# Performance work log

Measured on AMD Instinct MI355X. Metric: run time of the kernel, lower is better.

## Reference

```python
import jax, jax.numpy as jnp
import numpy as np

NUM_HEAD = 16
FEAT_DIM = 1024
HEAD_DIM = FEAT_DIM // NUM_HEAD  # 64
MAX_SEQ_LEN = 2048
BATCH = 2


def setup_inputs() -> dict:
    key = jax.random.key(0)
    ks = jax.random.split(key, 6)
    x = jax.random.normal(ks[0], (BATCH, MAX_SEQ_LEN, FEAT_DIM), dtype=jnp.float32)
    # xavier_uniform: limit = sqrt(6/(fan_in+fan_out)); torch Linear weight is [out, in]
    def xavier(k, out_f, in_f):
        lim = float(np.sqrt(6.0 / (in_f + out_f)))
        return jax.random.uniform(k, (out_f, in_f), dtype=jnp.float32, minval=-lim, maxval=lim)
    W1 = xavier(ks[1], HEAD_DIM, HEAD_DIM)          # attn_mlp[0].weight
    b1 = jnp.zeros((HEAD_DIM,), dtype=jnp.float32)
    W2 = xavier(ks[2], MAX_SEQ_LEN, HEAD_DIM)       # attn_mlp[2].weight
    b2 = jnp.zeros((MAX_SEQ_LEN,), dtype=jnp.float32)
    Wv = xavier(ks[3], FEAT_DIM, FEAT_DIM)          # value_linear.weight (no bias)
    Wo = xavier(ks[4], FEAT_DIM, FEAT_DIM)          # output_linear.weight (no bias)
    return {"x": x, "W1": W1, "b1": b1, "W2": W2, "b2": b2, "Wv": Wv, "Wo": Wo}


def _split_head(t):
    b, n, _ = t.shape
    return t.reshape(b, n, NUM_HEAD, HEAD_DIM).transpose(0, 2, 1, 3)  # [b,h,n,d]


def reference(x, W1, b1, W2, b2, Wv, Wo):
    # value projection (dropout is identity in eval / p=0)
    value = x @ Wv.T                                   # [b,n,F]
    vh = _split_head(value)                            # [b,h,n,d]
    xh = _split_head(x)                                # [b,h,n,d]
    # per-head MLP -> dense attention logits [b,h,n,max_seq_len]
    hid = jax.nn.relu(jnp.einsum('bhnd,ed->bhne', xh, W1) + b1)
    logits = jnp.einsum('bhne,me->bhnm', hid, W2) + b2
    attn = jax.nn.softmax(logits, axis=-1)             # [b,h,n,m]
    out_h = jnp.einsum('bhnm,bhmd->bhnd', attn, vh)    # m == seq_len
    b_, h_, n_, d_ = out_h.shape
    out = out_h.transpose(0, 2, 1, 3).reshape(b_, n_, FEAT_DIM)
    return out @ Wo.T
```

## Files before the change

### kernel.cpp

```cpp
#include <hip/hip_runtime.h>
#include <hip/hip_bf16.h>
#include <math.h>
#include <stdint.h>


typedef __attribute__((ext_vector_type(8))) short bf16x8;
typedef __attribute__((ext_vector_type(4))) float f32x4;
typedef __attribute__((ext_vector_type(16))) float f32x16;

#define LOG2E 1.4426950408889634f

__device__ __forceinline__ unsigned short f2bf(float f) {
  union { float f; unsigned u; } v; v.f = f;
  unsigned r = v.u + 0x7FFFu + ((v.u >> 16) & 1u);
  return (unsigned short)(r >> 16);
}

__global__ __launch_bounds__(256) void prep_all(const float* __restrict__ x,
                                                const float* __restrict__ Wv,
                                                const float* __restrict__ Wo,
                                                const float* __restrict__ W2,
                                                const float* __restrict__ W1,
                                                const float* __restrict__ b2,
                                                unsigned short* __restrict__ xb,
                                                unsigned short* __restrict__ wvb,
                                                unsigned short* __restrict__ wob,
                                                unsigned short* __restrict__ w2b,
                                                unsigned short* __restrict__ w1b,
                                                float* __restrict__ b2l) {
  int bid = blockIdx.x;
  if (bid == 2048) {
    int i = threadIdx.x;
#pragma unroll
    for (int t = 0; t < 8; ++t) {
      int k = i * 8 + t;
      b2l[k] = b2[k] * LOG2E;
    }
    return;
  }
  int stride = 2048 * 256;
  for (int q = bid * 256 + threadIdx.x; q < 1606656; q += stride) {
    const float* s; unsigned short* d; int o;
    if (q < 1048576)      { s = x;  d = xb;  o = q; }
    else {
      int q2 = q - 1048576;
      if (q2 < 262144)      { s = Wv; d = wvb; o = q2; }
      else if (q2 < 524288) { s = Wo; d = wob; o = q2 - 262144; }
      else if (q2 < 557056) { s = W2; d = w2b; o = q2 - 524288; }
      else                  { s = W1; d = w1b; o = q2 - 557056; }
    }
    float4 v = *(const float4*)(s + (size_t)o * 4);
    uint2 u;
    u.x = (unsigned)f2bf(v.x) | ((unsigned)f2bf(v.y) << 16);
    u.y = (unsigned)f2bf(v.z) | ((unsigned)f2bf(v.w) << 16);
    *(uint2*)(d + (size_t)o * 4) = u;
  }
}

__device__ __forceinline__ void stage64(const char* g, size_t ldbytes, char* lds,
                                        int w, int lane) {
#pragma unroll
  for (int t = 0; t < 2; ++t) {
    int row  = w * 16 + t * 8 + (lane >> 3);
    int csrc = (lane & 7) ^ (lane >> 3);
    const char* src = g + (size_t)row * ldbytes + (csrc << 4);
    char* dst = lds + ((w * 2 + t) << 10);
    __builtin_amdgcn_global_load_lds((const __attribute__((address_space(1))) void*)src,
                                     (__attribute__((address_space(3))) void*)dst,
                                     16, 0, 0);
  }
}

__device__ __forceinline__ void stage8(const char* g, size_t ldbytes, char* lds_,
                                       int w, int lane) {
  int row  = w * 8 + (lane >> 3);
  int csrc = (lane & 7) ^ (lane >> 3);
  const char* src = g + (size_t)row * ldbytes + (csrc << 4);
  char* dst = lds_ + (w << 10);
  __builtin_amdgcn_global_load_lds((const __attribute__((address_space(1))) void*)src,
                                   (__attribute__((address_space(3))) void*)dst,
                                   16, 0, 0);
}

__device__ __forceinline__ bf16x8 rdfrag32(const char* lds, int row, int chunk) {
  int c = chunk ^ (row & 7);
  return *(const bf16x8*)(lds + row * 128 + (c << 4));
}

__device__ __forceinline__ f32x16 loadb16(const float* p) {
  f32x16 r;
#pragma unroll
  for (int qd = 0; qd < 4; ++qd) {
    float4 v = *(const float4*)(p + qd * 8);
    r[qd * 4 + 0] = v.x; r[qd * 4 + 1] = v.y; r[qd * 4 + 2] = v.z; r[qd * 4 + 3] = v.w;
  }
  return r;
}

__device__ __forceinline__ bf16x8 pk_swap(float r0, float r1, float r2, float r3,
                                          float r4, float r5, float r6, float r7) {
  unsigned a, b, c, d;
  asm("v_cvt_pk_bf16_f32 %0, %1, %2" : "=v"(a) : "v"(r0), "v"(r1));
  asm("v_cvt_pk_bf16_f32 %0, %1, %2" : "=v"(b) : "v"(r4), "v"(r5));
  asm("v_cvt_pk_bf16_f32 %0, %1, %2" : "=v"(c) : "v"(r2), "v"(r3));
  asm("v_cvt_pk_bf16_f32 %0, %1, %2" : "=v"(d) : "v"(r6), "v"(r7));
  asm("v_permlane32_swap_b32 %0, %1" : "+v"(a), "+v"(b));
  asm("v_permlane32_swap_b32 %0, %1" : "+v"(c), "+v"(d));
  union { unsigned u[4]; bf16x8 v; } r;
  r.u[0] = a; r.u[1] = c; r.u[2] = b; r.u[3] = d;
  return r.v;
}

template<int MODE>
__global__ __launch_bounds__(256) void gemm12864(const unsigned short* __restrict__ A,
                                                 const unsigned short* __restrict__ B,
                                                 void* __restrict__ C, int K) {
  __shared__ __attribute__((aligned(16))) char As[2][16384];
  __shared__ __attribute__((aligned(16))) char Bs[2][8192];
  int tid = threadIdx.x, w = tid >> 6, lane = tid & 63;
  int l31 = lane & 31, hi = lane >> 5;
  int wr = w >> 1, wc = w & 1;
  int bm = blockIdx.x, bn = blockIdx.y;
  const char* Ab = (const char*)A + (size_t)bm * 128 * (K * 2);
  const char* Bb = (const char*)B + (size_t)bn * 64 * (K * 2);
  size_t ld = (size_t)K * 2;

  f32x16 acc0 = {}, acc1 = {};
  stage64(Ab, ld, As[0], w, lane);
  stage64(Ab + 64 * ld, ld, As[0] + 8192, w, lane);
  stage64(Bb, ld, Bs[0], w, lane);
  __syncthreads();

  int nst = K >> 6;
  for (int kk = 0; kk < nst; ++kk) {
    int cur = kk & 1;
    if (kk + 1 < nst) {
      const char* An = Ab + (size_t)(kk + 1) * 128;
      const char* Bn = Bb + (size_t)(kk + 1) * 128;
      stage64(An, ld, As[cur ^ 1], w, lane);
      stage64(An + 64 * ld, ld, As[cur ^ 1] + 8192, w, lane);
      stage64(Bn, ld, Bs[cur ^ 1], w, lane);
    }
    __builtin_amdgcn_s_setprio(1);
#pragma unroll
    for (int ks = 0; ks < 4; ++ks) {
      bf16x8 a0 = rdfrag32(As[cur], wr * 64 + l31, ks * 2 + hi);
      bf16x8 a1 = rdfrag32(As[cur], wr * 64 + 32 + l31, ks * 2 + hi);
      bf16x8 b0 = rdfrag32(Bs[cur], wc * 32 + l31, ks * 2 + hi);
      acc0 = __builtin_amdgcn_mfma_f32_32x32x16_bf16(a0, b0, acc0, 0, 0, 0);
      acc1 = __builtin_amdgcn_mfma_f32_32x32x16_bf16(a1, b0, acc1, 0, 0, 0);
    }
    __builtin_amdgcn_s_setprio(0);
    __syncthreads();
  }

  if (MODE == 0) {
    unsigned short* vt = (unsigned short*)C;
    int d = wc * 32 + l31;
#pragma unroll
    for (int i = 0; i < 2; ++i) {
      f32x16 a = i ? acc1 : acc0;
      int rowb = bm * 128 + wr * 64 + i * 32;
#pragma unroll
      for (int qd = 0; qd < 4; ++qd) {
        int m0 = rowb + qd * 8 + hi * 4;
        int bb = m0 >> 11, n = m0 & 2047;
        int r0 = qd * 4;
        uint2 u;
        u.x = (unsigned)f2bf(a[r0]) | ((unsigned)f2bf(a[r0 + 1]) << 16);
        u.y = (unsigned)f2bf(a[r0 + 2]) | ((unsigned)f2bf(a[r0 + 3]) << 16);
        *(uint2*)(vt + ((size_t)((bb * 16 + bn) * 64 + d)) * 2048 + n) = u;
      }
    }
  } else {
    float* Cf = (float*)C;
    int rb = bm * 128 + wr * 64, cb = bn * 64 + wc * 32;
#pragma unroll
    for (int r = 0; r < 16; ++r) {
      int row = (r & 3) + 8 * (r >> 2) + 4 * hi;
      Cf[(size_t)(rb + row) * 1024 + cb + l31]      = acc0[r];
      Cf[(size_t)(rb + 32 + row) * 1024 + cb + l31] = acc1[r];
    }
  }
}

__global__ __launch_bounds__(512, 2) void flash_kernel(const unsigned short* __restrict__ xb,
                                                       const unsigned short* __restrict__ w1b,
                                                       const float* __restrict__ b1,
                                                       const unsigned short* __restrict__ w2b,
                                                       const float* __restrict__ b2l,
                                                       const unsigned short* __restrict__ vt,
                                                       unsigned short* __restrict__ aout) {
  __shared__ __attribute__((aligned(16))) char lds[65536];
  int tid = threadIdx.x, w = tid >> 6, lane = tid & 63;
  int wq = w & 3, grp = w >> 2;
  int l31 = lane & 31, hi = lane >> 5;
  int f = blockIdx.x;
  int swz = ((f & 7) << 6) | (f >> 3);
  int qt = swz & 15, bh = swz >> 4;
  int b = bh >> 4, h = bh & 15;

  const char* px = (const char*)(xb + ((size_t)(b * 2048 + qt * 128)) * 1024 + h * 64);
  stage8(px, 2048, lds, w, lane);
  stage8(px + (size_t)64 * 2048, 2048, lds + 8192, w, lane);
  stage8((const char*)w1b, 128, lds + 32768, w, lane);
  __syncthreads();

  f32x16 h0 = loadb16(b1 + hi * 4);
  f32x16 h1 = loadb16(b1 + 32 + hi * 4);
  {
    const char* xt = lds + (wq >> 1) * 8192;
    int xr = (wq & 1) * 32 + l31;
#pragma unroll
    for (int ks = 0; ks < 4; ++ks) {
      bf16x8 xf = rdfrag32(xt, xr, ks * 2 + hi);
      bf16x8 wf0 = rdfrag32(lds + 32768, l31, ks * 2 + hi);
      h0 = __builtin_amdgcn_mfma_f32_32x32x16_bf16(wf0, xf, h0, 0, 0, 0);
      bf16x8 wf1 = rdfrag32(lds + 32768, 32 + l31, ks * 2 + hi);
      h1 = __builtin_amdgcn_mfma_f32_32x32x16_bf16(wf1, xf, h1, 0, 0, 0);
    }
  }
#pragma unroll
  for (int i = 0; i < 16; ++i) {
    h0[i] = fmaxf(h0[i], 0.f) * LOG2E;
    h1[i] = fmaxf(h1[i], 0.f) * LOG2E;
  }
  bf16x8 qb[4];
  qb[0] = pk_swap(h0[0], h0[1], h0[2], h0[3], h0[4], h0[5], h0[6], h0[7]);
  qb[1] = pk_swap(h0[8], h0[9], h0[10], h0[11], h0[12], h0[13], h0[14], h0[15]);
  qb[2] = pk_swap(h1[0], h1[1], h1[2], h1[3], h1[4], h1[5], h1[6], h1[7]);
  qb[3] = pk_swap(h1[8], h1[9], h1[10], h1[11], h1[12], h1[13], h1[14], h1[15]);
  __syncthreads();

  const char* vtb = (const char*)vt + (size_t)bh * 64 * 4096;
#pragma unroll
  for (int t = 0; t < 4; ++t) {
    stage8((const char*)w2b + (size_t)t * 8192, 128, lds + t * 8192, w, lane);
    stage8(vtb + (size_t)t * 128, 4096, lds + 32768 + t * 8192, w, lane);
  }
  f32x16 oA = {}, oB = {};
  float lrs0 = 0.f, lrs1 = 0.f, lrs2 = 0.f, lrs3 = 0.f;
  __syncthreads();

  for (int s = 0; s < 16; ++s) {
    int mt = 2 * s + grp;
    const char* Kc = lds + (mt & 3) * 8192;
    const char* Vc = lds + 32768 + (mt & 3) * 8192;

    f32x16 s0, s1;
#pragma unroll
    for (int qd = 0; qd < 4; ++qd) {
      f32x4 p0 = *(const f32x4*)(b2l + mt * 64 + qd * 8 + hi * 4);
      f32x4 p1 = *(const f32x4*)(b2l + mt * 64 + 32 + qd * 8 + hi * 4);
#pragma unroll
      for (int j = 0; j < 4; ++j) {
        s0[qd * 4 + j] = p0[j];
        s1[qd * 4 + j] = p1[j];
      }
    }
    __builtin_amdgcn_s_setprio(1);
#pragma unroll
    for (int kt = 0; kt < 4; ++kt) {
      bf16x8 kf0 = rdfrag32(Kc, l31, kt * 2 + hi);
      s0 = __builtin_amdgcn_mfma_f32_32x32x16_bf16(kf0, qb[kt], s0, 0, 0, 0);
      bf16x8 kf1 = rdfrag32(Kc, 32 + l31, kt * 2 + hi);
      s1 = __builtin_amdgcn_mfma_f32_32x32x16_bf16(kf1, qb[kt], s1, 0, 0, 0);
    }
    __builtin_amdgcn_s_setprio(0);
#pragma unroll
    for (int i = 0; i < 16; ++i) {
      float t0, t1;
      asm("v_exp_f32 %0, %1" : "=v"(t0) : "v"(s0[i]));
      asm("v_exp_f32 %0, %1" : "=v"(t1) : "v"(s1[i]));
      s0[i] = t0; s1[i] = t1;
      if ((i & 3) == 0) { lrs0 += t0; lrs0 += t1; }
      else if ((i & 3) == 1) { lrs1 += t0; lrs1 += t1; }
      else if ((i & 3) == 2) { lrs2 += t0; lrs2 += t1; }
      else { lrs3 += t0; lrs3 += t1; }
    }
    bf16x8 pa0 = pk_swap(s0[0], s0[1], s0[2], s0[3], s0[4], s0[5], s0[6], s0[7]);
    bf16x8 pa1 = pk_swap(s0[8], s0[9], s0[10], s0[11], s0[12], s0[13], s0[14], s0[15]);
    bf16x8 pa2 = pk_swap(s1[0], s1[1], s1[2], s1[3], s1[4], s1[5], s1[6], s1[7]);
    bf16x8 pa3 = pk_swap(s1[8], s1[9], s1[10], s1[11], s1[12], s1[13], s1[14], s1[15]);
    __builtin_amdgcn_s_setprio(1);
    {
      bf16x8 vf;
      vf = rdfrag32(Vc, l31, 0 + hi);
      oA = __builtin_amdgcn_mfma_f32_32x32x16_bf16(pa0, vf, oA, 0, 0, 0);
      vf = rdfrag32(Vc, 32 + l31, 0 + hi);
      oB = __builtin_amdgcn_mfma_f32_32x32x16_bf16(pa0, vf, oB, 0, 0, 0);
      vf = rdfrag32(Vc, l31, 2 + hi);
      oA = __builtin_amdgcn_mfma_f32_32x32x16_bf16(pa1, vf, oA, 0, 0, 0);
      vf = rdfrag32(Vc, 32 + l31, 2 + hi);
      oB = __builtin_amdgcn_mfma_f32_32x32x16_bf16(pa1, vf, oB, 0, 0, 0);
      vf = rdfrag32(Vc, l31, 4 + hi);
      oA = __builtin_amdgcn_mfma_f32_32x32x16_bf16(pa2, vf, oA, 0, 0, 0);
      vf = rdfrag32(Vc, 32 + l31, 4 + hi);
      oB = __builtin_amdgcn_mfma_f32_32x32x16_bf16(pa2, vf, oB, 0, 0, 0);
      vf = rdfrag32(Vc, l31, 6 + hi);
      oA = __builtin_amdgcn_mfma_f32_32x32x16_bf16(pa3, vf, oA, 0, 0, 0);
      vf = rdfrag32(Vc, 32 + l31, 6 + hi);
      oB = __builtin_amdgcn_mfma_f32_32x32x16_bf16(pa3, vf, oB, 0, 0, 0);
    }
    __builtin_amdgcn_s_setprio(0);
    __syncthreads();
    if (s < 14) {
      int t0 = 2 * s + 4, t1 = 2 * s + 5;
      stage8((const char*)w2b + (size_t)t0 * 8192, 128, lds + (t0 & 3) * 8192, w, lane);
      stage8(vtb + (size_t)t0 * 128, 4096, lds + 32768 + (t0 & 3) * 8192, w, lane);
      stage8((const char*)w2b + (size_t)t1 * 8192, 128, lds + (t1 & 3) * 8192, w, lane);
      stage8(vtb + (size_t)t1 * 128, 4096, lds + 32768 + (t1 & 3) * 8192, w, lane);
    }
  }

  float lpart = (lrs0 + lrs1) + (lrs2 + lrs3);
  float* comb = (float*)lds;
  if (grp == 1) {
    float* cb = comb + (wq * 64 + lane) * 36;
#pragma unroll
    for (int i = 0; i < 4; ++i) {
      *(float4*)(cb + i * 4)      = make_float4(oA[i*4], oA[i*4+1], oA[i*4+2], oA[i*4+3]);
      *(float4*)(cb + 16 + i * 4) = make_float4(oB[i*4], oB[i*4+1], oB[i*4+2], oB[i*4+3]);
    }
    cb[32] = lpart;
  }
  __syncthreads();
  if (grp == 0) {
    float* cb = comb + (wq * 64 + lane) * 36;
#pragma unroll
    for (int i = 0; i < 4; ++i) {
      float4 a = *(const float4*)(cb + i * 4);
      float4 bq = *(const float4*)(cb + 16 + i * 4);
      oA[i*4] += a.x; oA[i*4+1] += a.y; oA[i*4+2] += a.z; oA[i*4+3] += a.w;
      oB[i*4] += bq.x; oB[i*4+1] += bq.y; oB[i*4+2] += bq.z; oB[i*4+3] += bq.w;
    }
    float l = lpart + cb[32];
    l += __shfl_xor(l, 32);
    float inv = 1.f / l;
    float iv[16];
#pragma unroll
    for (int r = 0; r < 16; ++r)
      iv[r] = __shfl(inv, (r & 3) + 8 * (r >> 2) + 4 * hi);
    int nb = qt * 128 + wq * 32;
#pragma unroll
    for (int r = 0; r < 16; ++r) {
      int ql = (r & 3) + 8 * (r >> 2) + 4 * hi;
      size_t off = ((size_t)(b * 2048 + nb + ql)) * 1024 + h * 64 + l31;
      aout[off]      = f2bf(oA[r] * iv[r]);
      aout[off + 32] = f2bf(oB[r] * iv[r]);
    }
  }
}

extern "C" void kernel_launch(void* const* d_in, const int* in_sizes, int n_in,
                              void* d_out, int out_size, void* d_ws, size_t ws_size,
                              hipStream_t stream) {
  (void)in_sizes; (void)n_in; (void)out_size; (void)ws_size;
  const float* x  = (const float*)d_in[0];
  const float* W1 = (const float*)d_in[1];
  const float* b1 = (const float*)d_in[2];
  const float* W2 = (const float*)d_in[3];
  const float* b2 = (const float*)d_in[4];
  const float* Wv = (const float*)d_in[5];
  const float* Wo = (const float*)d_in[6];
  float* out = (float*)d_out;

  char* ws = (char*)d_ws;
  unsigned short* xb   = (unsigned short*)(ws);
  unsigned short* wvb  = (unsigned short*)(ws +  8388608);
  unsigned short* wob  = (unsigned short*)(ws + 10485760);
  unsigned short* w2b  = (unsigned short*)(ws + 12582912);
  unsigned short* w1b  = (unsigned short*)(ws + 12845056);
  float*          b2l  = (float*)         (ws + 12853248);
  unsigned short* vt   = (unsigned short*)(ws + 21233664);
  unsigned short* aout = (unsigned short*)(ws + 29622272);

  prep_all<<<2049, 256, 0, stream>>>(x, Wv, Wo, W2, W1, b2,
                                     xb, wvb, wob, w2b, w1b, b2l);

  gemm12864<0><<<dim3(32, 16), 256, 0, stream>>>(xb, wvb, (void*)vt, 1024);
  flash_kernel<<<512, 512, 0, stream>>>(xb, w1b, b1, w2b, b2l, vt, aout);
  gemm12864<1><<<dim3(32, 16), 256, 0, stream>>>(aout, wob, (void*)out, 1024);
}
```

Before: 94.22 us.

## Drop split-K wave groups in flash kernel; use 4-wave blocks with double buffering

The flash kernel drops from 8 waves (two groups splitting the key tiles, merged through LDS at the end) to 4 waves per block, each handling all 32 key tiles. Staging becomes a 2-deep double buffer prefetching the next W2/V tile at the top of each iteration, and the b2 bias row is staged into LDS once instead of read from global memory each tile. The aim is to remove the cross-group combine and its barrier, cut LDS to 40KB to allow more resident blocks, and overlap loads with compute. In exchange each block has half the waves and twice as many serial iterations, with a barrier per tile.

```diff
diff --git a/kernel.cpp b/kernel.cpp
--- a/kernel.cpp
+++ b/kernel.cpp
@@ -71,17 +71,6 @@
   }
 }
 
-__device__ __forceinline__ void stage8(const char* g, size_t ldbytes, char* lds_,
-                                       int w, int lane) {
-  int row  = w * 8 + (lane >> 3);
-  int csrc = (lane & 7) ^ (lane >> 3);
-  const char* src = g + (size_t)row * ldbytes + (csrc << 4);
-  char* dst = lds_ + (w << 10);
-  __builtin_amdgcn_global_load_lds((const __attribute__((address_space(1))) void*)src,
-                                   (__attribute__((address_space(3))) void*)dst,
-                                   16, 0, 0);
-}
-
 __device__ __forceinline__ bf16x8 rdfrag32(const char* lds, int row, int chunk) {
   int c = chunk ^ (row & 7);
   return *(const bf16x8*)(lds + row * 128 + (c << 4));
@@ -184,16 +173,15 @@
   }
 }
 
-__global__ __launch_bounds__(512, 2) void flash_kernel(const unsigned short* __restrict__ xb,
+__global__ __launch_bounds__(256, 4) void flash_kernel(const unsigned short* __restrict__ xb,
                                                        const unsigned short* __restrict__ w1b,
                                                        const float* __restrict__ b1,
                                                        const unsigned short* __restrict__ w2b,
                                                        const float* __restrict__ b2l,
                                                        const unsigned short* __restrict__ vt,
                                                        unsigned short* __restrict__ aout) {
-  __shared__ __attribute__((aligned(16))) char lds[65536];
+  __shared__ __attribute__((aligned(16))) char lds[40960];
   int tid = threadIdx.x, w = tid >> 6, lane = tid & 63;
-  int wq = w & 3, grp = w >> 2;
   int l31 = lane & 31, hi = lane >> 5;
   int f = blockIdx.x;
   int swz = ((f & 7) << 6) | (f >> 3);
@@ -201,22 +189,30 @@
   int b = bh >> 4, h = bh & 15;
 
   const char* px = (const char*)(xb + ((size_t)(b * 2048 + qt * 128)) * 1024 + h * 64);
-  stage8(px, 2048, lds, w, lane);
-  stage8(px + (size_t)64 * 2048, 2048, lds + 8192, w, lane);
-  stage8((const char*)w1b, 128, lds + 32768, w, lane);
+  stage64(px, 2048, lds, w, lane);
+  stage64(px + (size_t)64 * 2048, 2048, lds + 8192, w, lane);
+  stage64((const char*)w1b, 128, lds + 16384, w, lane);
+#pragma unroll
+  for (int t = 0; t < 2; ++t) {
+    const char* src = (const char*)b2l + ((w * 2 + t) << 10) + (lane << 4);
+    char* dst = lds + 32768 + ((w * 2 + t) << 10);
+    __builtin_amdgcn_global_load_lds((const __attribute__((address_space(1))) void*)src,
+                                     (__attribute__((address_space(3))) void*)dst,
+                                     16, 0, 0);
+  }
   __syncthreads();
 
   f32x16 h0 = loadb16(b1 + hi * 4);
   f32x16 h1 = loadb16(b1 + 32 + hi * 4);
   {
-    const char* xt = lds + (wq >> 1) * 8192;
-    int xr = (wq & 1) * 32 + l31;
+    const char* xt = lds + (w >> 1) * 8192;
+    int xr = (w & 1) * 32 + l31;
 #pragma unroll
     for (int ks = 0; ks < 4; ++ks) {
       bf16x8 xf = rdfrag32(xt, xr, ks * 2 + hi);
-      bf16x8 wf0 = rdfrag32(lds + 32768, l31, ks * 2 + hi);
+      bf16x8 wf0 = rdfrag32(lds + 16384, l31, ks * 2 + hi);
       h0 = __builtin_amdgcn_mfma_f32_32x32x16_bf16(wf0, xf, h0, 0, 0, 0);
-      bf16x8 wf1 = rdfrag32(lds + 32768, 32 + l31, ks * 2 + hi);
+      bf16x8 wf1 = rdfrag32(lds + 16384, 32 + l31, ks * 2 + hi);
       h1 = __builtin_amdgcn_mfma_f32_32x32x16_bf16(wf1, xf, h1, 0, 0, 0);
     }
   }
@@ -233,25 +229,28 @@
   __syncthreads();
 
   const char* vtb = (const char*)vt + (size_t)bh * 64 * 4096;
-#pragma unroll
-  for (int t = 0; t < 4; ++t) {
-    stage8((const char*)w2b + (size_t)t * 8192, 128, lds + t * 8192, w, lane);
-    stage8(vtb + (size_t)t * 128, 4096, lds + 32768 + t * 8192, w, lane);
-  }
+  stage64((const char*)w2b, 128, lds, w, lane);
+  stage64(vtb, 4096, lds + 8192, w, lane);
   f32x16 oA = {}, oB = {};
   float lrs0 = 0.f, lrs1 = 0.f, lrs2 = 0.f, lrs3 = 0.f;
+  const float* bl = (const float*)(lds + 32768);
   __syncthreads();
 
-  for (int s = 0; s < 16; ++s) {
-    int mt = 2 * s + grp;
-    const char* Kc = lds + (mt & 3) * 8192;
-    const char* Vc = lds + 32768 + (mt & 3) * 8192;
+  for (int mt = 0; mt < 32; ++mt) {
+    int cur = mt & 1;
+    const char* Kc = lds + (cur << 14);
+    const char* Vc = Kc + 8192;
+    if (mt < 31) {
+      char* nx = lds + ((cur ^ 1) << 14);
+      stage64((const char*)w2b + (size_t)(mt + 1) * 8192, 128, nx, w, lane);
+      stage64(vtb + (size_t)(mt + 1) * 128, 4096, nx + 8192, w, lane);
+    }
 
     f32x16 s0, s1;
 #pragma unroll
     for (int qd = 0; qd < 4; ++qd) {
-      f32x4 p0 = *(const f32x4*)(b2l + mt * 64 + qd * 8 + hi * 4);
-      f32x4 p1 = *(const f32x4*)(b2l + mt * 64 + 32 + qd * 8 + hi * 4);
+      f32x4 p0 = *(const f32x4*)(bl + mt * 64 + qd * 8 + hi * 4);
+      f32x4 p1 = *(const f32x4*)(bl + mt * 64 + 32 + qd * 8 + hi * 4);
 #pragma unroll
       for (int j = 0; j < 4; ++j) {
         s0[qd * 4 + j] = p0[j];
@@ -304,51 +303,22 @@
     }
     __builtin_amdgcn_s_setprio(0);
     __syncthreads();
-    if (s < 14) {
-      int t0 = 2 * s + 4, t1 = 2 * s + 5;
-      stage8((const char*)w2b + (size_t)t0 * 8192, 128, lds + (t0 & 3) * 8192, w, lane);
-      stage8(vtb + (size_t)t0 * 128, 4096, lds + 32768 + (t0 & 3) * 8192, w, lane);
-      stage8((const char*)w2b + (size_t)t1 * 8192, 128, lds + (t1 & 3) * 8192, w, lane);
-      stage8(vtb + (size_t)t1 * 128, 4096, lds + 32768 + (t1 & 3) * 8192, w, lane);
-    }
-  }
-
-  float lpart = (lrs0 + lrs1) + (lrs2 + lrs3);
-  float* comb = (float*)lds;
-  if (grp == 1) {
-    float* cb = comb + (wq * 64 + lane) * 36;
-#pragma unroll
-    for (int i = 0; i < 4; ++i) {
-      *(float4*)(cb + i * 4)      = make_float4(oA[i*4], oA[i*4+1], oA[i*4+2], oA[i*4+3]);
-      *(float4*)(cb + 16 + i * 4) = make_float4(oB[i*4], oB[i*4+1], oB[i*4+2], oB[i*4+3]);
-    }
-    cb[32] = lpart;
-  }
-  __syncthreads();
-  if (grp == 0) {
-    float* cb = comb + (wq * 64 + lane) * 36;
-#pragma unroll
-    for (int i = 0; i < 4; ++i) {
-      float4 a = *(const float4*)(cb + i * 4);
-      float4 bq = *(const float4*)(cb + 16 + i * 4);
-      oA[i*4] += a.x; oA[i*4+1] += a.y; oA[i*4+2] += a.z; oA[i*4+3] += a.w;
-      oB[i*4] += bq.x; oB[i*4+1] += bq.y; oB[i*4+2] += bq.z; oB[i*4+3] += bq.w;
-    }
-    float l = lpart + cb[32];
-    l += __shfl_xor(l, 32);
-    float inv = 1.f / l;
-    float iv[16];
-#pragma unroll
-    for (int r = 0; r < 16; ++r)
-      iv[r] = __shfl(inv, (r & 3) + 8 * (r >> 2) + 4 * hi);
-    int nb = qt * 128 + wq * 32;
-#pragma unroll
-    for (int r = 0; r < 16; ++r) {
-      int ql = (r & 3) + 8 * (r >> 2) + 4 * hi;
-      size_t off = ((size_t)(b * 2048 + nb + ql)) * 1024 + h * 64 + l31;
-      aout[off]      = f2bf(oA[r] * iv[r]);
-      aout[off + 32] = f2bf(oB[r] * iv[r]);
-    }
+  }
+
+  float l = (lrs0 + lrs1) + (lrs2 + lrs3);
+  l += __shfl_xor(l, 32);
+  float inv = 1.f / l;
+  float iv[16];
+#pragma unroll
+  for (int r = 0; r < 16; ++r)
+    iv[r] = __shfl(inv, (r & 3) + 8 * (r >> 2) + 4 * hi);
+  int nb = qt * 128 + w * 32;
+#pragma unroll
+  for (int r = 0; r < 16; ++r) {
+    int ql = (r & 3) + 8 * (r >> 2) + 4 * hi;
+    size_t off = ((size_t)(b * 2048 + nb + ql)) * 1024 + h * 64 + l31;
+    aout[off]      = f2bf(oA[r] * iv[r]);
+    aout[off + 32] = f2bf(oB[r] * iv[r]);
   }
 }
 
@@ -379,6 +349,6 @@
                                      xb, wvb, wob, w2b, w1b, b2l);
 
   gemm12864<0><<<dim3(32, 16), 256, 0, stream>>>(xb, wvb, (void*)vt, 1024);
-  flash_kernel<<<512, 512, 0, stream>>>(xb, w1b, b1, w2b, b2l, vt, aout);
+  flash_kernel<<<512, 256, 0, stream>>>(xb, w1b, b1, w2b, b2l, vt, aout);
   gemm12864<1><<<dim3(32, 16), 256, 0, stream>>>(aout, wob, (void*)out, 1024);
 }
```

Measured after the change: 93.98 us. No clear change (-0.3%).
